# Kernel tuning notes

Hardware: AMD Instinct MI355X
Metric: run time of the kernel (lower is better)

Reference implementation:

```python
import jax, jax.numpy as jnp
import numpy as np
from jax import lax

K = 3          # kernel (patch size)
D = 64         # MPO bond dimension
F = K * K      # feature dim per patch (k^2 * C, C=1)
S = F          # output-index spacing inside each SMPO
OUT = 10       # final output dimension
B = 128        # batch size
H = 81         # image height = width
SIGMA = 1e-3   # 'random_eye' noise scale


def patch_embed(x, k=K):
    """squeeze_image + trigonometric embedding.
    x: (B, h, w) -> unit vectors (B, N, 2) with N=(h/k)*(w/k).
    Each k*k patch row is embedded as the L2-normalized mean of
    [cos(pi/2 x), sin(pi/2 x)] over its k^2 features."""
    b, h, w = x.shape
    p = x.reshape(b, h // k, k, w // k, k).transpose(0, 1, 3, 2, 4)
    p = p.reshape(b, (h // k) * (w // k), k * k)
    ang = 0.5 * jnp.pi * p
    v = jnp.stack([jnp.cos(ang).mean(-1), jnp.sin(ang).mean(-1)], axis=-1)
    return v / jnp.linalg.norm(v, axis=-1, keepdims=True)


def smpo_layer(v, W_out, W_mid):
    """Spaced MPO applied to a product-state MPS, read out per output site.
    v:      (B, n, 2)  input site vectors (n = J*S sites, output at every S-th)
    W_out:  (J, D, D, 2, F)  output-site tensors (identity baseline baked in)
    W_mid:  (J, S-1, D, D, 2) non-output site tensors; effective matrix is
            M = I + einsum('bp,dep->bde', v, W) ('random_eye' init).
    Output row j = L_j . A_j(v) . R_j where L/R are left/right chain
    environments with the other output indices closed with ones.
    Returns (B, J, F)."""
    b, n, _ = v.shape
    J = W_out.shape[0]
    s = n // J
    eye = jnp.eye(D, dtype=v.dtype)
    vg = v.reshape(b, J, s, 2)
    v_out = vg[:, :, 0, :].transpose(1, 0, 2)        # (J, B, 2)
    v_mid = vg[:, :, 1:, :].transpose(1, 2, 0, 3)    # (J, S-1, B, 2)

    def left_step(l, xs):
        A, vo, Wm, vm = xs
        Lj = l                                       # env left of output site j
        l = jnp.einsum('bd,bp,depf->be', l, vo, A)   # Abar (f summed = ones closure)
        for t in range(s - 1):
            M = eye + jnp.einsum('bp,dep->bde', vm[t], Wm[t])
            l = jnp.einsum('bd,bde->be', l, M)
        return l, Lj

    def right_step(r, xs):
        A, vo, Wm, vm = xs
        for t in reversed(range(s - 1)):
            M = eye + jnp.einsum('bp,dep->bde', vm[t], Wm[t])
            r = jnp.einsum('bde,be->bd', M, r)
        Rj = r                                       # env right of output site j
        r = jnp.einsum('bp,depf,be->bd', vo, A, r)
        return r, Rj

    bnd = jnp.zeros((b, D), v.dtype).at[:, 0].set(1.0)  # bond-1 boundary
    xs = (W_out, v_out, W_mid, v_mid)
    _, L = lax.scan(jax.checkpoint(left_step), bnd, xs)
    _, R = lax.scan(jax.checkpoint(right_step), bnd, xs, reverse=True)
    return jnp.einsum('jbd,jdepf,jbp,jbe->bjf', L, W_out, v_out, R)


def final_layer(x, A0, W_mid):
    """Final SMPO (spacing = n, single output index at site 0), fully
    contracted left-to-right. x: (B, n) -> (B, OUT)."""
    ang = 0.5 * jnp.pi * x
    v = jnp.stack([jnp.cos(ang), jnp.sin(ang)], axis=-1)   # (B, n, 2)
    eye = jnp.eye(D, dtype=x.dtype)
    u = jnp.einsum('bp,epo->beo', v[:, 0], A0[0])          # left boundary e0

    def step(u, xs):
        Wm, vm = xs
        M = eye + jnp.einsum('bp,dep->bde', vm, Wm)
        return jnp.einsum('bdo,bde->beo', u, M), None

    u, _ = lax.scan(jax.checkpoint(step), u, (W_mid, v[:, 1:].transpose(1, 0, 2)))
    return u[:, 0, :]                                      # right boundary e0


def setup_inputs() -> dict:
    key = jax.random.key(0)
    ks = jax.random.split(key, 7)
    eyeD = np.eye(D, dtype=np.float32)

    def wout(k, J):  # identity baseline + noise ('random_eye')
        base = jnp.asarray((0.8 / F) * eyeD[:, :, None, None])
        return base + SIGMA * jax.random.normal(k, (J, D, D, 2, F), jnp.float32)

    def wmid(k, J):
        return SIGMA * jax.random.normal(k, (J, S - 1, D, D, 2), jnp.float32)

    x = jax.random.uniform(ks[0], (B, H, H, 1), jnp.float32)
    Wout0 = wout(ks[1], 81)
    Wmid0 = wmid(ks[2], 81)
    Wout1 = wout(ks[3], 9)
    Wmid1 = wmid(ks[4], 9)
    A0f = jnp.asarray(0.1 * eyeD[:, :, None, None]) + SIGMA * jax.random.normal(
        ks[5], (D, D, 2, OUT), jnp.float32)
    WmidF = SIGMA * jax.random.normal(ks[6], (80, D, D, 2), jnp.float32)
    return {"x": x, "Wout0": Wout0, "Wmid0": Wmid0, "Wout1": Wout1,
            "Wmid1": Wmid1, "A0f": A0f, "WmidF": WmidF}


def reference(x, Wout0, Wmid0, Wout1, Wmid1, A0f, WmidF):
    v0 = patch_embed(x[..., 0])                    # (B, 729, 2)
    h1 = smpo_layer(v0, Wout0, Wmid0)              # (B, 81, 9)
    v1 = patch_embed(h1.reshape(-1, 27, 27))       # (B, 81, 2)
    h2 = smpo_layer(v1, Wout1, Wmid1)              # (B, 9, 9)
    return final_layer(h2.reshape(-1, 81), A0f, WmidF)  # (B, 10)
```

## Files before the change

kernel.cpp:

```cpp
#include <hip/hip_runtime.h>
#include <cstdint>
#include <cstddef>


typedef float    f32x16 __attribute__((ext_vector_type(16)));
typedef _Float16 f16x8  __attribute__((ext_vector_type(8)));
typedef __fp16   fp16x2 __attribute__((ext_vector_type(2)));
typedef _Float16 h2_t   __attribute__((ext_vector_type(2)));
typedef const void __attribute__((address_space(1))) gas_t;
typedef void       __attribute__((address_space(3))) las_t;

union U16  { uint4 u; f16x8 h; };
union B16u { uint32_t u[4]; f16x8 h; };
union H2U  { fp16x2 h; uint32_t u; };

__device__ __forceinline__ uint32_t pkf16(float a, float b){
  H2U z; z.h = __builtin_amdgcn_cvt_pkrtz(a, b); return z.u;
}
__device__ __forceinline__ uint32_t pkmul(uint32_t a, uint32_t b){
  H2U x, y, r; x.u = a; y.u = b;
  r.h = x.h * y.h; return r.u;
}
__device__ __forceinline__ uint32_t packh2(float a, float b){
  union { _Float16 h[2]; uint32_t u; } z;
  z.h[0] = (_Float16)a; z.h[1] = (_Float16)b; return z.u;
}
__device__ __forceinline__ float fdot2f(uint32_t wa, uint32_t wb, float acc){
  union U { uint32_t u; h2_t h; };
  U a, b; a.u = wa; b.u = wb;
  return __builtin_amdgcn_fdot2(a.h, b.h, acc, false);
}

#define REC 17408

__global__ void k_build(const float* __restrict__ Wmid, const float* __restrict__ Wout,
                        char* __restrict__ S, int J, int n, int dirR){
  int tid = blockIdx.x*256 + threadIdx.x;
  if (tid >= n*4096) return;
  int gt = tid >> 12, r = tid & 4095;
  int f = r >> 8, ln = (r >> 2) & 63, dw = r & 3;
  int s = f >> 1, m = f & 1;
  int row = m*32 + (ln & 31);
  int kb = s*16 + (ln >> 5)*8 + dw*2;
  int p = kb >> 6, q = kb & 63;
  int jj = gt/9, pos = gt - jj*9;
  int j = dirR ? (J-1-jj) : jj;
  int outs = dirR ? 8 : 0;
  float w[2];
  #pragma unroll
  for (int k2 = 0; k2 < 2; ++k2){
    int qq = q + k2;
    int d = dirR ? row : qq;
    int e = dirR ? qq : row;
    float val;
    if (pos == outs){
      const float* src = Wout + ((((size_t)j*64 + d)*64 + e)*2 + p)*9;
      val = 0.f;
      #pragma unroll
      for (int ff = 0; ff < 9; ++ff) val += src[ff];
      if (d == e) val -= 0.8f;
    } else {
      int mi = dirR ? (7 - pos) : (pos - 1);
      val = Wmid[((((size_t)j*8 + mi)*64 + d)*64 + e)*2 + p];
    }
    w[k2] = val;
  }
  uint32_t* S32 = (uint32_t*)(S + (size_t)gt*REC);
  S32[f*256 + ln*4 + dw] = packh2(w[0]*256.f, w[1]*256.f);
}

__global__ void k_buildF(const float* __restrict__ Wm, char* __restrict__ S){
  int tid = blockIdx.x*256 + threadIdx.x;
  if (tid >= 80*4096) return;
  int gt = tid >> 12, r = tid & 4095;
  int f = r >> 8, ln = (r >> 2) & 63, dw = r & 3;
  int s = f >> 1, m = f & 1;
  int row = m*32 + (ln & 31);
  int kb = s*16 + (ln >> 5)*8 + dw*2;
  int p = kb >> 6, q = kb & 63;
  float w[2];
  #pragma unroll
  for (int k2 = 0; k2 < 2; ++k2){
    int d = q + k2, e = row;
    w[k2] = Wm[(((size_t)gt*64 + d)*64 + e)*2 + p];
  }
  uint32_t* S32 = (uint32_t*)(S + (size_t)gt*REC);
  S32[f*256 + ln*4 + dw] = packh2(w[0]*256.f, w[1]*256.f);
}

__global__ void k_vrec(const float2* __restrict__ v, char* __restrict__ S,
                       int n, int nv, int mode){
  int tid = blockIdx.x*256 + threadIdx.x;
  if (tid >= n*128) return;
  int gt = tid >> 7, b = tid & 127;
  int site = (mode == 0) ? gt : (mode == 1) ? (n-1-gt) : (gt+1);
  *(float2*)(S + (size_t)gt*REC + 16384 + b*8) = v[(size_t)b*nv + site];
}

__global__ void k_embed(const float* __restrict__ img, int Wd, int PG,
                        float2* __restrict__ outv){
  int tid = blockIdx.x*256 + threadIdx.x;
  int NP = PG*PG;
  if (tid >= 128*NP) return;
  int b = tid / NP, s = tid - b*NP;
  int pi = s / PG, pj = s - pi*PG;
  const float* base = img + (size_t)b*Wd*Wd + (size_t)(3*pi)*Wd + 3*pj;
  float cs = 0.f, sn = 0.f;
  #pragma unroll
  for (int r = 0; r < 3; ++r){
    #pragma unroll
    for (int c = 0; c < 3; ++c){
      float x = base[r*Wd + c];
      float s_, c_; sincosf(1.5707963267948966f*x, &s_, &c_);
      cs += c_; sn += s_;
    }
  }
  cs *= (1.f/9.f); sn *= (1.f/9.f);
  float rn = rsqrtf(cs*cs + sn*sn);
  float2 v; v.x = cs*rn; v.y = sn*rn;
  outv[tid] = v;
}

__device__ __forceinline__ void stage17(const char* g, char* l){
  #pragma unroll
  for (int i = 0; i < 17; ++i)
    __builtin_amdgcn_global_load_lds((gas_t*)(const void*)(g + i*1024),
                                     (las_t*)(void*)(l + i*1024), 16, 0, 0);
}

#define MKBASE(acc, bd) do { \
  uint32_t P0 = pkf16(acc[0],acc[1]),  P1 = pkf16(acc[2],acc[3]); \
  uint32_t P2 = pkf16(acc[4],acc[5]),  P3 = pkf16(acc[6],acc[7]); \
  uint32_t Q0 = (uint32_t)__shfl_xor((int)P0, 32); \
  uint32_t Q1 = (uint32_t)__shfl_xor((int)P1, 32); \
  uint32_t Q2 = (uint32_t)__shfl_xor((int)P2, 32); \
  uint32_t Q3 = (uint32_t)__shfl_xor((int)P3, 32); \
  bd[0] = hlo ? P0 : Q2;  bd[1] = hlo ? P1 : Q3; \
  bd[2] = hlo ? Q0 : P2;  bd[3] = hlo ? Q1 : P3; \
  uint32_t R0 = pkf16(acc[8],acc[9]),   R1 = pkf16(acc[10],acc[11]); \
  uint32_t R2 = pkf16(acc[12],acc[13]), R3 = pkf16(acc[14],acc[15]); \
  uint32_t T0 = (uint32_t)__shfl_xor((int)R0, 32); \
  uint32_t T1 = (uint32_t)__shfl_xor((int)R1, 32); \
  uint32_t T2 = (uint32_t)__shfl_xor((int)R2, 32); \
  uint32_t T3 = (uint32_t)__shfl_xor((int)R3, 32); \
  bd[4] = hlo ? R0 : T2;  bd[5] = hlo ? R1 : T3; \
  bd[6] = hlo ? T0 : R2;  bd[7] = hlo ? T1 : R3; \
} while(0)

#define MFMA8(slotp) do { \
  const uint4* fr_ = (const uint4*)(slotp); \
  _Pragma("unroll") \
  for (int s_ = 0; s_ < 8; ++s_){ \
    const int sl_ = s_ & 3; \
    const uint32_t* bb_ = (sl_ < 2) ? bd0 : bd1; \
    const int off_ = (sl_ & 1)*4; \
    const uint32_t scl_ = (s_ < 4) ? px : py; \
    B16u bs_; \
    _Pragma("unroll") \
    for (int dw_ = 0; dw_ < 4; ++dw_) bs_.u[dw_] = pkmul(bb_[off_+dw_], scl_); \
    U16 fa0_, fa1_; \
    fa0_.u = fr_[(2*s_)*64 + ln]; \
    fa1_.u = fr_[(2*s_+1)*64 + ln]; \
    acc0 = __builtin_amdgcn_mfma_f32_32x32x16_f16(fa0_.h, bs_.h, acc0, 0, 0, 0); \
    acc1 = __builtin_amdgcn_mfma_f32_32x32x16_f16(fa1_.h, bs_.h, acc1, 0, 0, 0); \
  } \
} while(0)

#define PROD_SLOOP(buf) do { \
  const uint4* fr = (const uint4*)(buf); \
  _Pragma("unroll") \
  for (int s = 0; s < 8; ++s){ \
    const int sl = s & 3; \
    const uint32_t scl = (s < 4) ? px : py; \
    const int off = (sl & 1)*4; \
    U16 f0, f1; \
    f0.u = fr[(2*s)*64 + ln]; \
    f1.u = fr[(2*s+1)*64 + ln]; \
    { \
      const uint32_t* bb = (sl < 2) ? bl0 : bh0; \
      B16u bs; \
      _Pragma("unroll") \
      for (int dw = 0; dw < 4; ++dw) bs.u[dw] = pkmul(bb[off+dw], scl); \
      a00 = __builtin_amdgcn_mfma_f32_32x32x16_f16(f0.h, bs.h, a00, 0, 0, 0); \
      a10 = __builtin_amdgcn_mfma_f32_32x32x16_f16(f1.h, bs.h, a10, 0, 0, 0); \
    } \
    { \
      const uint32_t* bb = (sl < 2) ? bl1 : bh1; \
      B16u bs; \
      _Pragma("unroll") \
      for (int dw = 0; dw < 4; ++dw) bs.u[dw] = pkmul(bb[off+dw], scl); \
      a01 = __builtin_amdgcn_mfma_f32_32x32x16_f16(f0.h, bs.h, a01, 0, 0, 0); \
      a11 = __builtin_amdgcn_mfma_f32_32x32x16_f16(f1.h, bs.h, a11, 0, 0, 0); \
    } \
  } \
} while(0)

#define PROD_INIT_I() do { \
  _Pragma("unroll") \
  for (int i = 0; i < 16; ++i){ a00[i]=0.f; a01[i]=0.f; a10[i]=0.f; a11[i]=0.f; } \
  if (((i32 >> 2) & 1) == h){ \
    int rr0 = (i32 & 3) | ((i32 >> 3) << 2); \
    _Pragma("unroll") \
    for (int rr = 0; rr < 16; ++rr) \
      if (rr == rr0){ a00[rr] = 1.f; a11[rr] = 1.f; } \
  } \
} while(0)

#define PROD_WRITEOUT(ob, diagc) do { \
  _Pragma("unroll") \
  for (int x = 0; x < 2; ++x){ \
    _Pragma("unroll") \
    for (int y = 0; y < 2; ++y){ \
      const f32x16& A = (x==0) ? (y==0 ? a00 : a01) : (y==0 ? a10 : a11); \
      int C = y*32 + i32; \
      _Pragma("unroll") \
      for (int r = 0; r < 16; ++r){ \
        int R = x*32 + (r & 3) + 8*(r >> 2) + 4*h; \
        float val = (A[r] - ((R == C) ? (diagc) : 0.f))*256.f; \
        float oth = __shfl_xor(val, 1); \
        if (!(ln & 1)){ \
          uint32_t dwv = packh2(val, oth); \
          *(uint32_t*)((ob) + R*128 + ((C*2) ^ ((R & 7) << 4))) = dwv; \
        } \
      } \
    } \
  } \
} while(0)

__global__ __launch_bounds__(512, 1) void k_prod(
    const char* __restrict__ sL, const char* __restrict__ sR,
    const float2* __restrict__ v, char* __restrict__ Tn, char* __restrict__ Wn,
    int J){
  __shared__ __align__(16) char lds[2][16384];
  const int ln = threadIdx.x & 63, w = threadIdx.x >> 6;
  const int wid = (blockIdx.x & 7)*(J*4) + (blockIdx.x >> 3);
  const int bg = wid & 15;
  const int pair = wid >> 4;
  const int dir = pair & 1, j = pair >> 1;
  const int b = bg*8 + w;
  const bool hlo = (ln < 32);
  const int h = ln >> 5, i32 = ln & 31;
  const float INV = 1.f/256.f;
  const char* stream = dir ? sR : sL;
  const int n = J*9;

  float2 vv[9];
  {
    const float2* vbase = v + (size_t)b*n + j*9;
    #pragma unroll
    for (int t = 0; t < 9; ++t) vv[t] = vbase[dir ? (9 - t) : t];
  }
  const float alphaC = (dir && j == J-1) ? 1.0f : 0.8f*(vv[0].x + vv[0].y);
  if (dir && j == J-1){ vv[0].x = 0.f; vv[0].y = 0.f; }

  auto gtf = [&](int t) -> int {
    int g = dir ? ((J-2-j)*9 + 8 + t) : (j*9 + t);
    return g < 0 ? 0 : g;
  };
  auto stage = [&](int t, int sl){
    const char* g0 = stream + (size_t)gtf(t)*REC + (size_t)(2*w)*1024 + (size_t)ln*16;
    __builtin_amdgcn_global_load_lds((gas_t*)(const void*)g0,
                                     (las_t*)(void*)(lds[sl] + 2*w*1024), 16, 0, 0);
    __builtin_amdgcn_global_load_lds((gas_t*)(const void*)(g0 + 1024),
                                     (las_t*)(void*)(lds[sl] + (2*w+1)*1024), 16, 0, 0);
  };

  f32x16 a00, a01, a10, a11;
  PROD_INIT_I();

  stage(0, 0);
  #pragma unroll
  for (int t = 0; t < 9; ++t){
    asm volatile("s_waitcnt vmcnt(0)" ::: "memory");
    __builtin_amdgcn_s_barrier();
    if (t < 8) stage(t+1, (t+1) & 1);
    uint32_t px = pkf16(vv[t].x*INV, vv[t].x*INV);
    uint32_t py = pkf16(vv[t].y*INV, vv[t].y*INV);
    uint32_t bl0[8], bh0[8], bl1[8], bh1[8];
    MKBASE(a00, bl0); MKBASE(a10, bh0);
    MKBASE(a01, bl1); MKBASE(a11, bh1);
    if (t == 0){
      #pragma unroll
      for (int i = 0; i < 16; ++i){
        a00[i] *= alphaC; a01[i] *= alphaC; a10[i] *= alphaC; a11[i] *= alphaC;
      }
    }
    PROD_SLOOP(lds[t & 1]);
  }

  char* ob = (dir ? Wn : Tn) + ((size_t)b*J + j)*8192;
  PROD_WRITEOUT(ob, alphaC);
}

__global__ __launch_bounds__(512, 1) void k_prodF(
    const char* __restrict__ sF, const float2* __restrict__ vF,
    char* __restrict__ GF){
  __shared__ __align__(16) char lds[2][16384];
  const int ln = threadIdx.x & 63, w = threadIdx.x >> 6;
  const int wid = (blockIdx.x & 7)*20 + (blockIdx.x >> 3);
  const int bg = wid & 15, g = wid >> 4;
  const int b = bg*8 + w;
  const bool hlo = (ln < 32);
  const int h = ln >> 5, i32 = ln & 31;
  const float INV = 1.f/256.f;

  float2 vv[8];
  {
    const float2* vbase = vF + (size_t)b*81 + g*8 + 1;
    #pragma unroll
    for (int t = 0; t < 8; ++t) vv[t] = vbase[t];
  }
  auto stage = [&](int t, int sl){
    const char* g0 = sF + (size_t)(g*8 + t)*REC + (size_t)(2*w)*1024 + (size_t)ln*16;
    __builtin_amdgcn_global_load_lds((gas_t*)(const void*)g0,
                                     (las_t*)(void*)(lds[sl] + 2*w*1024), 16, 0, 0);
    __builtin_amdgcn_global_load_lds((gas_t*)(const void*)(g0 + 1024),
                                     (las_t*)(void*)(lds[sl] + (2*w+1)*1024), 16, 0, 0);
  };

  f32x16 a00, a01, a10, a11;
  PROD_INIT_I();

  stage(0, 0);
  #pragma unroll
  for (int t = 0; t < 8; ++t){
    asm volatile("s_waitcnt vmcnt(0)" ::: "memory");
    __builtin_amdgcn_s_barrier();
    if (t < 7) stage(t+1, (t+1) & 1);
    uint32_t px = pkf16(vv[t].x*INV, vv[t].x*INV);
    uint32_t py = pkf16(vv[t].y*INV, vv[t].y*INV);
    uint32_t bl0[8], bh0[8], bl1[8], bh1[8];
    MKBASE(a00, bl0); MKBASE(a10, bh0);
    MKBASE(a01, bl1); MKBASE(a11, bh1);
    PROD_SLOOP(lds[t & 1]);
  }

  char* ob = GF + ((size_t)b*10 + g)*8192;
  PROD_WRITEOUT(ob, 1.0f);
}

__global__ __launch_bounds__(64, 1) void k_gscan(
    const char* __restrict__ Tn, const char* __restrict__ Wn,
    const float2* __restrict__ v,
    float* __restrict__ Lout, float* __restrict__ Rout, int J){
  __shared__ __align__(16) char slot[2][8192];
  __shared__ __align__(16) float2 vvs[81];
  __shared__ __align__(16) uint32_t pk32[32];
  const int ln = threadIdx.x;
  const int dir = blockIdx.x >> 7;
  const int b = blockIdx.x & 127;
  const float INV = 1.f/256.f;
  const char* P = (dir ? Wn : Tn) + (size_t)b*J*8192;

  for (int g = ln; g < J; g += 64) vvs[g] = v[(size_t)b*(J*9) + (size_t)g*9];

  auto JD = [&](int g){ return dir ? (J-1-g) : g; };
  auto stage8 = [&](int jx, int sl){
    const char* g0 = P + (size_t)jx*8192 + (size_t)ln*16;
    #pragma unroll
    for (int i = 0; i < 8; ++i)
      __builtin_amdgcn_global_load_lds((gas_t*)(const void*)(g0 + i*1024),
                                       (las_t*)(void*)(slot[sl] + i*1024), 16, 0, 0);
  };

  stage8(JD(0), 0);
  asm volatile("s_waitcnt vmcnt(0)" ::: "memory");

  float st = (ln == 0) ? 1.f : 0.f;
  const uint32_t swz = (uint32_t)(ln & 7) << 4;

  #pragma unroll 1
  for (int g = 0; g < J; ++g){
    const int j = JD(g);
    if (!dir) Lout[((size_t)j*128 + b)*64 + ln] = st;
    int gn = g + 1; if (gn > J-1) gn = J-1;
    stage8(JD(gn), (g+1) & 1);
    asm volatile("s_waitcnt vmcnt(8)" ::: "memory");

    float c;
    if (dir) c = (j < J-1) ? 0.8f*(vvs[j+1].x + vvs[j+1].y) : 1.0f;
    else     c = 0.8f*(vvs[j].x + vvs[j].y);

    {
      float o = __shfl_xor(st, 1);
      pk32[ln>>1] = (ln & 1) ? packh2(o, st) : packh2(st, o);
    }
    const char* sp = slot[g & 1] + (size_t)ln*128;
    const uint4* lp = (const uint4*)pk32;
    float acc = 0.f;
    #pragma unroll
    for (int m = 0; m < 8; ++m){
      uint4 q = lp[m];
      uint4 ww = *(const uint4*)(sp + ((m*16) ^ swz));
      acc = fdot2f(ww.x, q.x, acc); acc = fdot2f(ww.y, q.y, acc);
      acc = fdot2f(ww.z, q.z, acc); acc = fdot2f(ww.w, q.w, acc);
    }
    st = c*st + acc*INV;
    if (dir) Rout[((size_t)j*128 + b)*64 + ln] = st;
  }
}

__global__ __launch_bounds__(64, 1) void k_fscan(
    const char* __restrict__ GF, const float* __restrict__ A0f,
    const float2* __restrict__ vF, float* __restrict__ outp){
  __shared__ __align__(16) char slot[2][8192];
  __shared__ __align__(16) uint32_t pk[10][32];
  const int ln = threadIdx.x;
  const int b = blockIdx.x;
  const float INV = 1.f/256.f;
  const char* P = GF + (size_t)b*10*8192;

  float2 v0 = vF[(size_t)b*81];
  float u[10];
  #pragma unroll
  for (int o = 0; o < 10; ++o)
    u[o] = v0.x*A0f[(ln*2+0)*10 + o] + v0.y*A0f[(ln*2+1)*10 + o];

  auto stage8 = [&](int g, int sl){
    const char* g0 = P + (size_t)g*8192 + (size_t)ln*16;
    #pragma unroll
    for (int i = 0; i < 8; ++i)
      __builtin_amdgcn_global_load_lds((gas_t*)(const void*)(g0 + i*1024),
                                       (las_t*)(void*)(slot[sl] + i*1024), 16, 0, 0);
  };

  stage8(0, 0);
  const uint32_t swz = (uint32_t)(ln & 7) << 4;

  #pragma unroll 1
  for (int g = 0; g < 10; ++g){
    if (g < 9){
      stage8(g+1, (g+1) & 1);
      asm volatile("s_waitcnt vmcnt(8)" ::: "memory");
    } else {
      asm volatile("s_waitcnt vmcnt(0)" ::: "memory");
    }
    #pragma unroll
    for (int o = 0; o < 10; ++o){
      float ot = __shfl_xor(u[o], 1);
      pk[o][ln>>1] = (ln & 1) ? packh2(ot, u[o]) : packh2(u[o], ot);
    }
    const char* sp = slot[g & 1] + (size_t)ln*128;
    uint4 wr[8];
    #pragma unroll
    for (int m = 0; m < 8; ++m) wr[m] = *(const uint4*)(sp + ((m*16) ^ swz));
    #pragma unroll
    for (int o = 0; o < 10; ++o){
      const uint4* lp = (const uint4*)pk[o];
      float acc = 0.f;
      #pragma unroll
      for (int m = 0; m < 8; ++m){
        uint4 q = lp[m];
        acc = fdot2f(wr[m].x, q.x, acc); acc = fdot2f(wr[m].y, q.y, acc);
        acc = fdot2f(wr[m].z, q.z, acc); acc = fdot2f(wr[m].w, q.w, acc);
      }
      u[o] += acc*INV;
    }
  }
  if (ln == 0){
    #pragma unroll
    for (int o = 0; o < 10; ++o) outp[(size_t)b*10 + o] = u[o];
  }
}

__global__ __launch_bounds__(64, 1) void k_scan_m(
    const char* __restrict__ sL, const char* __restrict__ sR,
    float* __restrict__ Lout, float* __restrict__ Rout, int J, int n){
  __shared__ __align__(16) char lds[4*REC];
  const int ln = threadIdx.x;
  const int wg = blockIdx.x;
  const int dir = wg >> 2;
  const int colbase = (wg & 3)*32;
  const char* stream = dir ? sR : sL;
  float* Sout = dir ? Rout : Lout;
  const int outs = dir ? 8 : 0;
  const int b = colbase + (ln & 31);
  const bool hlo = (ln < 32);
  const int h4 = (ln >> 5)*4;
  const float INV = 1.f/256.f;

  f32x16 acc0, acc1;
  #pragma unroll
  for (int i = 0; i < 16; ++i){ acc0[i] = 0.f; acc1[i] = 0.f; }
  if (hlo) acc0[0] = 1.f;

  const char* gsrc = stream + (size_t)ln*16;
  stage17(gsrc,           lds);
  stage17(gsrc + REC,     lds + REC);
  stage17(gsrc + 2*REC,   lds + 2*REC);

  int pos = 0, jj = 0;
  for (int t = 0; t < n; ++t){
    asm volatile("s_waitcnt vmcnt(34)" ::: "memory");
    const char* slot = lds + (size_t)(t & 3)*REC;
    float2 vv = *(const float2*)(slot + 16384 + b*8);
    int tn = t + 3; if (tn > n-1) tn = n-1;
    stage17(gsrc + (size_t)tn*REC, lds + (size_t)(tn & 3)*REC);

    uint32_t px = pkf16(vv.x*INV, vv.x*INV);
    uint32_t py = pkf16(vv.y*INV, vv.y*INV);
    uint32_t bd0[8], bd1[8];
    MKBASE(acc0, bd0);
    MKBASE(acc1, bd1);

    if (pos == outs){
      int jdx = dir ? (J-1-jj) : jj;
      float* dst = Sout + ((size_t)jdx*128 + b)*64;
      #pragma unroll
      for (int q = 0; q < 4; ++q){
        float4 f0; f0.x = acc0[4*q]; f0.y = acc0[4*q+1]; f0.z = acc0[4*q+2]; f0.w = acc0[4*q+3];
        *(float4*)(dst + 8*q + h4) = f0;
        float4 f1; f1.x = acc1[4*q]; f1.y = acc1[4*q+1]; f1.z = acc1[4*q+2]; f1.w = acc1[4*q+3];
        *(float4*)(dst + 32 + 8*q + h4) = f1;
      }
      float alpha = 0.8f*(vv.x + vv.y);
      #pragma unroll
      for (int i = 0; i < 16; ++i){ acc0[i] *= alpha; acc1[i] *= alpha; }
    }

    MFMA8(slot);

    ++pos; if (pos == 9){ pos = 0; ++jj; }
  }
}

__global__ __launch_bounds__(64, 1) void k_final_m(
    const char* __restrict__ sF, const float* __restrict__ A0f,
    const float2* __restrict__ vF, float* __restrict__ outp){
  __shared__ __align__(16) char lds[4*REC];
  const int ln = threadIdx.x;
  const int wg = blockIdx.x;
  const int o = wg >> 2;
  const int b = (wg & 3)*32 + (ln & 31);
  const bool hlo = (ln < 32);
  const int h4 = (ln >> 5)*4;
  const float INV = 1.f/256.f;

  float2 v0 = vF[(size_t)b*81];
  f32x16 acc0, acc1;
  #pragma unroll
  for (int rg = 0; rg < 16; ++rg){
    int row0 = (rg & 3) + 8*(rg >> 2) + h4;
    acc0[rg] = v0.x*A0f[(row0*2+0)*10 + o] + v0.y*A0f[(row0*2+1)*10 + o];
    int row1 = row0 + 32;
    acc1[rg] = v0.x*A0f[(row1*2+0)*10 + o] + v0.y*A0f[(row1*2+1)*10 + o];
  }
  asm volatile("s_waitcnt vmcnt(0)" ::: "memory");

  const char* gsrc = sF + (size_t)ln*16;
  stage17(gsrc,         lds);
  stage17(gsrc + REC,   lds + REC);
  stage17(gsrc + 2*REC, lds + 2*REC);

  const int n = 80;
  for (int t = 0; t < n; ++t){
    asm volatile("s_waitcnt vmcnt(34)" ::: "memory");
    const char* slot = lds + (size_t)(t & 3)*REC;
    float2 vv = *(const float2*)(slot + 16384 + b*8);
    int tn = t + 3; if (tn > n-1) tn = n-1;
    stage17(gsrc + (size_t)tn*REC, lds + (size_t)(tn & 3)*REC);

    uint32_t px = pkf16(vv.x*INV, vv.x*INV);
    uint32_t py = pkf16(vv.y*INV, vv.y*INV);
    uint32_t bd0[8], bd1[8];
    MKBASE(acc0, bd0);
    MKBASE(acc1, bd1);
    MFMA8(slot);
  }
  if (hlo) outp[(size_t)b*10 + o] = acc0[0];
}

template<bool EMB>
__global__ __launch_bounds__(256) void k_out(
    const float* __restrict__ Wout, const float* __restrict__ Lbuf,
    const float* __restrict__ Rbuf, const float2* __restrict__ v, int n,
    float* __restrict__ hout, float2* __restrict__ vF){
  __shared__ float tile[8][64][20];
  __shared__ float Lsh[64][65];
  const int j = blockIdx.x, bh = blockIdx.y;
  const int q = threadIdx.x >> 6, bl = threadIdx.x & 63;
  const int b = bh*64 + bl;
  for (int idx = threadIdx.x; idx < 64*64; idx += 256){
    int r = idx >> 6, d = idx & 63;
    Lsh[r][d] = Lbuf[((size_t)j*128 + bh*64 + r)*64 + d];
  }
  float Rr[16];
  {
    const float4* Rp = (const float4*)(Rbuf + ((size_t)j*128 + b)*64 + q*16);
    #pragma unroll
    for (int i = 0; i < 4; ++i) ((float4*)Rr)[i] = Rp[i];
  }
  float acc[18];
  #pragma unroll
  for (int k = 0; k < 18; ++k) acc[k] = 0.f;
  __syncthreads();
  for (int c = 0; c < 8; ++c){
    #pragma unroll
    for (int k = 0; k < 2; ++k){
      int pi = threadIdx.x*2 + k;
      int d8 = pi >> 6, e = pi & 63;
      const float* src = Wout + ((size_t)(j*64 + c*8 + d8)*64 + e)*18;
      float* dst = &tile[d8][e][0];
      #pragma unroll
      for (int mm = 0; mm < 18; ++mm) dst[mm] = src[mm];
    }
    __syncthreads();
    #pragma unroll 1
    for (int d8 = 0; d8 < 8; ++d8){
      float lw = Lsh[bl][c*8 + d8];
      #pragma unroll
      for (int i = 0; i < 16; ++i){
        int e = q*16 + i;
        float wbe = lw * Rr[i];
        const float* tp = &tile[d8][e][0];
        float4 t0 = *(const float4*)(tp);
        float4 t1 = *(const float4*)(tp+4);
        float4 t2 = *(const float4*)(tp+8);
        float4 t3 = *(const float4*)(tp+12);
        float2 t4 = *(const float2*)(tp+16);
        acc[0]  += wbe*t0.x; acc[1]  += wbe*t0.y; acc[2]  += wbe*t0.z; acc[3]  += wbe*t0.w;
        acc[4]  += wbe*t1.x; acc[5]  += wbe*t1.y; acc[6]  += wbe*t1.z; acc[7]  += wbe*t1.w;
        acc[8]  += wbe*t2.x; acc[9]  += wbe*t2.y; acc[10] += wbe*t2.z; acc[11] += wbe*t2.w;
        acc[12] += wbe*t3.x; acc[13] += wbe*t3.y; acc[14] += wbe*t3.z; acc[15] += wbe*t3.w;
        acc[16] += wbe*t4.x; acc[17] += wbe*t4.y;
      }
    }
    __syncthreads();
  }
  float* red = &tile[0][0][0];
  #pragma unroll
  for (int k = 0; k < 18; ++k) red[((size_t)q*64 + bl)*20 + k] = acc[k];
  __syncthreads();
  if (q == 0){
    float s[18];
    #pragma unroll
    for (int k = 0; k < 18; ++k)
      s[k] = red[(size_t)bl*20+k] + red[(64+(size_t)bl)*20+k]
           + red[(128+(size_t)bl)*20+k] + red[(192+(size_t)bl)*20+k];
    float2 vo = v[(size_t)b*n + j*9];
    #pragma unroll
    for (int f = 0; f < 9; ++f){
      float val = vo.x*s[f] + vo.y*s[9+f];
      if (EMB){
        float s_, c_; sincosf(1.5707963267948966f*val, &s_, &c_);
        float2 e2; e2.x = c_; e2.y = s_;
        vF[(size_t)b*81 + j*9 + f] = e2;
      } else {
        hout[(size_t)b*729 + j*9 + f] = val;
      }
    }
  }
}

extern "C" void kernel_launch(void* const* d_in, const int* in_sizes, int n_in,
                              void* d_out, int out_size, void* d_ws, size_t ws_size,
                              hipStream_t stream){
  const float* x     = (const float*)d_in[0];
  const float* Wout0 = (const float*)d_in[1];
  const float* Wmid0 = (const float*)d_in[2];
  const float* Wout1 = (const float*)d_in[3];
  const float* Wmid1 = (const float*)d_in[4];
  const float* A0f   = (const float*)d_in[5];
  const float* WmidF = (const float*)d_in[6];
  float* outp = (float*)d_out;

  char* ws = (char*)d_ws;
  size_t off = 0;
  auto alloc = [&](size_t bytes) -> char* {
    char* p = ws + off;
    off = (off + bytes + 255) & ~(size_t)255;
    return p;
  };
  char* S0L = alloc((size_t)729*REC);
  char* S0R = alloc((size_t)729*REC);
  char* S1L = alloc((size_t)81*REC);
  char* S1R = alloc((size_t)81*REC);
  char* SF  = alloc((size_t)80*REC);
  float2* v0 = (float2*)alloc((size_t)128*729*8);
  float2* v1 = (float2*)alloc((size_t)128*81*8);
  float2* vF = (float2*)alloc((size_t)128*81*8);
  float* L0 = (float*)alloc((size_t)81*128*64*4);
  float* R0 = (float*)alloc((size_t)81*128*64*4);
  float* L1 = (float*)alloc((size_t)9*128*64*4);
  float* R1 = (float*)alloc((size_t)9*128*64*4);
  float* h1 = (float*)alloc((size_t)128*729*4);
  char* Tn1 = alloc((size_t)128*81*8192);
  char* Wn1 = alloc((size_t)128*81*8192);
  size_t need_r7 = off;
  char* Tn2 = alloc((size_t)128*9*8192);
  char* Wn2 = alloc((size_t)128*9*8192);
  char* GF  = alloc((size_t)128*10*8192);
  size_t need_full = off;
  bool full = (ws_size >= need_full);
  bool grp1 = (ws_size >= need_r7);
  (void)in_sizes; (void)n_in; (void)out_size;

  k_build <<<1296,  256, 0, stream>>>(Wmid1, Wout1, S1L, 9, 81, 0);
  k_build <<<1296,  256, 0, stream>>>(Wmid1, Wout1, S1R, 9, 81, 1);
  k_buildF<<<1280,  256, 0, stream>>>(WmidF, SF);
  k_build<<<11664, 256, 0, stream>>>(Wmid0, Wout0, S0L, 81, 729, 0);
  k_build<<<11664, 256, 0, stream>>>(Wmid0, Wout0, S0R, 81, 729, 1);

  k_embed<<<365, 256, 0, stream>>>(x, 81, 27, v0);
  if (grp1){
    k_prod <<<2592, 512, 0, stream>>>(S0L, S0R, v0, Tn1, Wn1, 81);
    k_gscan<<<256, 64, 0, stream>>>(Tn1, Wn1, v0, L0, R0, 81);
  } else {
    k_vrec <<<365, 256, 0, stream>>>(v0, S0L, 729, 729, 0);
    k_vrec <<<365, 256, 0, stream>>>(v0, S0R, 729, 729, 1);
    k_scan_m<<<8, 64, 0, stream>>>(S0L, S0R, L0, R0, 81, 729);
  }
  k_out<false><<<dim3(81,2), 256, 0, stream>>>(Wout0, L0, R0, v0, 729, h1, (float2*)nullptr);

  k_embed<<<41, 256, 0, stream>>>(h1, 27, 9, v1);
  if (full){
    k_prod <<<288, 512, 0, stream>>>(S1L, S1R, v1, Tn2, Wn2, 9);
    k_gscan<<<256, 64, 0, stream>>>(Tn2, Wn2, v1, L1, R1, 9);
  } else {
    k_vrec <<<41, 256, 0, stream>>>(v1, S1L, 81, 81, 0);
    k_vrec <<<41, 256, 0, stream>>>(v1, S1R, 81, 81, 1);
    k_scan_m<<<8, 64, 0, stream>>>(S1L, S1R, L1, R1, 9, 81);
  }
  k_out<true><<<dim3(9,2), 256, 0, stream>>>(Wout1, L1, R1, v1, 81, (float*)nullptr, vF);

  if (full){
    k_prodF<<<160, 512, 0, stream>>>(SF, vF, GF);
    k_fscan<<<128, 64, 0, stream>>>(GF, A0f, vF, outp);
  } else {
    k_vrec <<<40, 256, 0, stream>>>(vF, SF, 80, 81, 2);
    k_final_m<<<40, 64, 0, stream>>>(SF, A0f, vF, outp);
  }
}
```

Baseline: 546.5 us.

## Deepen prefetch pipelines in prod/scan kernels and split k_out over more blocks

The product kernels move from double to triple buffering with a prefetch distance of two. The serial scan kernels (k_gscan, k_fscan) move to four slots with a prefetch distance of three, so the waits no longer stall on the most recent load. The output-contraction kernel k_out now handles 32 batch rows per block instead of 64, doubling its grid and splitting the e-range eight ways, with a larger reduction step. The goal is to hide global-load latency in the latency-bound serial scans and to raise parallelism in k_out, at the cost of more LDS per block and some redundant tail loads.

```diff
diff --git a/kernel.cpp b/kernel.cpp
--- a/kernel.cpp
+++ b/kernel.cpp
@@ -231,7 +231,7 @@
     const char* __restrict__ sL, const char* __restrict__ sR,
     const float2* __restrict__ v, char* __restrict__ Tn, char* __restrict__ Wn,
     int J){
-  __shared__ __align__(16) char lds[2][16384];
+  __shared__ __align__(16) char lds[3][16384];
   const int ln = threadIdx.x & 63, w = threadIdx.x >> 6;
   const int wid = (blockIdx.x & 7)*(J*4) + (blockIdx.x >> 3);
   const int bg = wid & 15;
@@ -269,11 +269,15 @@
   PROD_INIT_I();
 
   stage(0, 0);
+  stage(1, 1);
   #pragma unroll
   for (int t = 0; t < 9; ++t){
-    asm volatile("s_waitcnt vmcnt(0)" ::: "memory");
+    asm volatile("s_waitcnt vmcnt(2)" ::: "memory");
     __builtin_amdgcn_s_barrier();
-    if (t < 8) stage(t+1, (t+1) & 1);
+    {
+      int tn = (t+2 > 8) ? 8 : (t+2);
+      stage(tn, (t+2) % 3);
+    }
     uint32_t px = pkf16(vv[t].x*INV, vv[t].x*INV);
     uint32_t py = pkf16(vv[t].y*INV, vv[t].y*INV);
     uint32_t bl0[8], bh0[8], bl1[8], bh1[8];
@@ -285,7 +289,7 @@
         a00[i] *= alphaC; a01[i] *= alphaC; a10[i] *= alphaC; a11[i] *= alphaC;
       }
     }
-    PROD_SLOOP(lds[t & 1]);
+    PROD_SLOOP(lds[t % 3]);
   }
 
   char* ob = (dir ? Wn : Tn) + ((size_t)b*J + j)*8192;
@@ -295,7 +299,7 @@
 __global__ __launch_bounds__(512, 1) void k_prodF(
     const char* __restrict__ sF, const float2* __restrict__ vF,
     char* __restrict__ GF){
-  __shared__ __align__(16) char lds[2][16384];
+  __shared__ __align__(16) char lds[3][16384];
   const int ln = threadIdx.x & 63, w = threadIdx.x >> 6;
   const int wid = (blockIdx.x & 7)*20 + (blockIdx.x >> 3);
   const int bg = wid & 15, g = wid >> 4;
@@ -322,17 +326,21 @@
   PROD_INIT_I();
 
   stage(0, 0);
+  stage(1, 1);
   #pragma unroll
   for (int t = 0; t < 8; ++t){
-    asm volatile("s_waitcnt vmcnt(0)" ::: "memory");
+    asm volatile("s_waitcnt vmcnt(2)" ::: "memory");
     __builtin_amdgcn_s_barrier();
-    if (t < 7) stage(t+1, (t+1) & 1);
+    {
+      int tn = (t+2 > 7) ? 7 : (t+2);
+      stage(tn, (t+2) % 3);
+    }
     uint32_t px = pkf16(vv[t].x*INV, vv[t].x*INV);
     uint32_t py = pkf16(vv[t].y*INV, vv[t].y*INV);
     uint32_t bl0[8], bh0[8], bl1[8], bh1[8];
     MKBASE(a00, bl0); MKBASE(a10, bh0);
     MKBASE(a01, bl1); MKBASE(a11, bh1);
-    PROD_SLOOP(lds[t & 1]);
+    PROD_SLOOP(lds[t % 3]);
   }
 
   char* ob = GF + ((size_t)b*10 + g)*8192;
@@ -343,7 +351,7 @@
     const char* __restrict__ Tn, const char* __restrict__ Wn,
     const float2* __restrict__ v,
     float* __restrict__ Lout, float* __restrict__ Rout, int J){
-  __shared__ __align__(16) char slot[2][8192];
+  __shared__ __align__(16) char slot[4][8192];
   __shared__ __align__(16) float2 vvs[81];
   __shared__ __align__(16) uint32_t pk32[32];
   const int ln = threadIdx.x;
@@ -364,7 +372,8 @@
   };
 
   stage8(JD(0), 0);
-  asm volatile("s_waitcnt vmcnt(0)" ::: "memory");
+  stage8(JD(1 < J-1 ? 1 : J-1), 1);
+  stage8(JD(2 < J-1 ? 2 : J-1), 2);
 
   float st = (ln == 0) ? 1.f : 0.f;
   const uint32_t swz = (uint32_t)(ln & 7) << 4;
@@ -372,10 +381,12 @@
   #pragma unroll 1
   for (int g = 0; g < J; ++g){
     const int j = JD(g);
+    asm volatile("s_waitcnt vmcnt(16)" ::: "memory");
     if (!dir) Lout[((size_t)j*128 + b)*64 + ln] = st;
-    int gn = g + 1; if (gn > J-1) gn = J-1;
-    stage8(JD(gn), (g+1) & 1);
-    asm volatile("s_waitcnt vmcnt(8)" ::: "memory");
+    {
+      int gn = (g+3 > J-1) ? (J-1) : (g+3);
+      stage8(JD(gn), (g+3) & 3);
+    }
 
     float c;
     if (dir) c = (j < J-1) ? 0.8f*(vvs[j+1].x + vvs[j+1].y) : 1.0f;
@@ -385,7 +396,7 @@
       float o = __shfl_xor(st, 1);
       pk32[ln>>1] = (ln & 1) ? packh2(o, st) : packh2(st, o);
     }
-    const char* sp = slot[g & 1] + (size_t)ln*128;
+    const char* sp = slot[g & 3] + (size_t)ln*128;
     const uint4* lp = (const uint4*)pk32;
     float acc = 0.f;
     #pragma unroll
@@ -403,7 +414,7 @@
 __global__ __launch_bounds__(64, 1) void k_fscan(
     const char* __restrict__ GF, const float* __restrict__ A0f,
     const float2* __restrict__ vF, float* __restrict__ outp){
-  __shared__ __align__(16) char slot[2][8192];
+  __shared__ __align__(16) char slot[4][8192];
   __shared__ __align__(16) uint32_t pk[10][32];
   const int ln = threadIdx.x;
   const int b = blockIdx.x;
@@ -425,22 +436,23 @@
   };
 
   stage8(0, 0);
+  stage8(1, 1);
+  stage8(2, 2);
   const uint32_t swz = (uint32_t)(ln & 7) << 4;
 
   #pragma unroll 1
   for (int g = 0; g < 10; ++g){
-    if (g < 9){
-      stage8(g+1, (g+1) & 1);
-      asm volatile("s_waitcnt vmcnt(8)" ::: "memory");
-    } else {
-      asm volatile("s_waitcnt vmcnt(0)" ::: "memory");
+    asm volatile("s_waitcnt vmcnt(16)" ::: "memory");
+    {
+      int gn = (g+3 > 9) ? 9 : (g+3);
+      stage8(gn, (g+3) & 3);
     }
     #pragma unroll
     for (int o = 0; o < 10; ++o){
       float ot = __shfl_xor(u[o], 1);
       pk[o][ln>>1] = (ln & 1) ? packh2(ot, u[o]) : packh2(u[o], ot);
     }
-    const char* sp = slot[g & 1] + (size_t)ln*128;
+    const char* sp = slot[g & 3] + (size_t)ln*128;
     uint4 wr[8];
     #pragma unroll
     for (int m = 0; m < 8; ++m) wr[m] = *(const uint4*)(sp + ((m*16) ^ swz));
@@ -576,19 +588,19 @@
     const float* __restrict__ Rbuf, const float2* __restrict__ v, int n,
     float* __restrict__ hout, float2* __restrict__ vF){
   __shared__ float tile[8][64][20];
-  __shared__ float Lsh[64][65];
+  __shared__ float Lsh[32][65];
   const int j = blockIdx.x, bh = blockIdx.y;
-  const int q = threadIdx.x >> 6, bl = threadIdx.x & 63;
-  const int b = bh*64 + bl;
-  for (int idx = threadIdx.x; idx < 64*64; idx += 256){
+  const int q = threadIdx.x >> 5, bl = threadIdx.x & 31;
+  const int b = bh*32 + bl;
+  for (int idx = threadIdx.x; idx < 32*64; idx += 256){
     int r = idx >> 6, d = idx & 63;
-    Lsh[r][d] = Lbuf[((size_t)j*128 + bh*64 + r)*64 + d];
-  }
-  float Rr[16];
+    Lsh[r][d] = Lbuf[((size_t)j*128 + bh*32 + r)*64 + d];
+  }
+  float Rr[8];
   {
-    const float4* Rp = (const float4*)(Rbuf + ((size_t)j*128 + b)*64 + q*16);
-    #pragma unroll
-    for (int i = 0; i < 4; ++i) ((float4*)Rr)[i] = Rp[i];
+    const float4* Rp = (const float4*)(Rbuf + ((size_t)j*128 + b)*64 + q*8);
+    ((float4*)Rr)[0] = Rp[0];
+    ((float4*)Rr)[1] = Rp[1];
   }
   float acc[18];
   #pragma unroll
@@ -609,8 +621,8 @@
     for (int d8 = 0; d8 < 8; ++d8){
       float lw = Lsh[bl][c*8 + d8];
       #pragma unroll
-      for (int i = 0; i < 16; ++i){
-        int e = q*16 + i;
+      for (int i = 0; i < 8; ++i){
+        int e = q*8 + i;
         float wbe = lw * Rr[i];
         const float* tp = &tile[d8][e][0];
         float4 t0 = *(const float4*)(tp);
@@ -629,14 +641,17 @@
   }
   float* red = &tile[0][0][0];
   #pragma unroll
-  for (int k = 0; k < 18; ++k) red[((size_t)q*64 + bl)*20 + k] = acc[k];
+  for (int k = 0; k < 18; ++k) red[((size_t)q*32 + bl)*20 + k] = acc[k];
   __syncthreads();
   if (q == 0){
     float s[18];
     #pragma unroll
-    for (int k = 0; k < 18; ++k)
-      s[k] = red[(size_t)bl*20+k] + red[(64+(size_t)bl)*20+k]
-           + red[(128+(size_t)bl)*20+k] + red[(192+(size_t)bl)*20+k];
+    for (int k = 0; k < 18; ++k){
+      float t = 0.f;
+      #pragma unroll
+      for (int g = 0; g < 8; ++g) t += red[((size_t)g*32 + bl)*20 + k];
+      s[k] = t;
+    }
     float2 vo = v[(size_t)b*n + j*9];
     #pragma unroll
     for (int f = 0; f < 9; ++f){
@@ -710,7 +725,7 @@
     k_vrec <<<365, 256, 0, stream>>>(v0, S0R, 729, 729, 1);
     k_scan_m<<<8, 64, 0, stream>>>(S0L, S0R, L0, R0, 81, 729);
   }
-  k_out<false><<<dim3(81,2), 256, 0, stream>>>(Wout0, L0, R0, v0, 729, h1, (float2*)nullptr);
+  k_out<false><<<dim3(81,4), 256, 0, stream>>>(Wout0, L0, R0, v0, 729, h1, (float2*)nullptr);
 
   k_embed<<<41, 256, 0, stream>>>(h1, 27, 9, v1);
   if (full){
@@ -721,7 +736,7 @@
     k_vrec <<<41, 256, 0, stream>>>(v1, S1R, 81, 81, 1);
     k_scan_m<<<8, 64, 0, stream>>>(S1L, S1R, L1, R1, 9, 81);
   }
-  k_out<true><<<dim3(9,2), 256, 0, stream>>>(Wout1, L1, R1, v1, 81, (float*)nullptr, vF);
+  k_out<true><<<dim3(9,4), 256, 0, stream>>>(Wout1, L1, R1, v1, 81, (float*)nullptr, vF);
 
   if (full){
     k_prodF<<<160, 512, 0, stream>>>(SF, vF, GF);
```

After: 502.2 us. 1.09x faster.
